# Kernel optimization log

Hardware: AMD Instinct MI355X
Metric: run time of the kernel (lower is better)

The kernel has to match this reference:

```python
import jax, jax.numpy as jnp
import numpy as np

NUM_K = 10
T = 1.0  # softmax temperature (forward default)


def setup_inputs() -> dict:
    key = jax.random.key(0)
    k1, k2, k3, k4 = jax.random.split(key, 4)
    B, H, P, D = 64, 12, 197, 64
    return {
        "att_s": jax.random.normal(k1, (B, H, P, P), dtype=jnp.float32),
        "att_t": jax.random.normal(k2, (B, H, P, P), dtype=jnp.float32),
        "v_s": jax.random.normal(k3, (B, H, P, D), dtype=jnp.float32),
        "v_t": jax.random.normal(k4, (B, H, P, D), dtype=jnp.float32),
    }


def _topk_masked_attend(att, v):
    # att: [B,H,P,P] logits, v: [B,H,P,D]
    a = jax.nn.softmax(att / T, axis=-1)
    # kth-largest value per row acts as the threshold (torch.topk semantics)
    margin = jax.lax.top_k(a, NUM_K)[0][..., -1]           # [B,H,P]
    a = a * (a >= margin[..., None])                        # keep top-k entries
    norm = a.sum(-1)                                        # [B,H,P]
    return jnp.einsum("bhpq,bhqd->bhpd", a, v) / norm[..., None]


def reference(att_s, att_t, v_s, v_t):
    out_s = _topk_masked_attend(att_s, v_s)
    out_t = _topk_masked_attend(att_t, v_t)
    # nn.MSELoss default reduction='mean'
    return jnp.mean(jnp.square(out_s - out_t))
```

## Files before the change

kernel.cpp:

```cpp
#include <hip/hip_runtime.h>
#include <cstdint>
#include <cfloat>

#define NK 10
constexpr int Pp   = 197;
constexpr int Dd   = 64;
constexpr int ROWS = 64 * 12 * 197;
constexpr int BLK  = 256;
constexpr int RPB  = 256;
constexpr int NBLK = ROWS / RPB;
constexpr int CH   = 32;
constexpr int NFULL = Pp / CH;
constexpr int TAIL  = Pp - NFULL * CH;
constexpr float INV_N = 1.0f / 9682944.0f;

__device__ __forceinline__ uint32_t fbits(float x) { return __float_as_uint(x); }
__device__ __forceinline__ float    bfl(uint32_t u) { return __uint_as_float(u); }

template <int CW>
__device__ __forceinline__ void consume_chunk(const float* __restrict__ trow,
                                              float a[NK]) {
#pragma unroll
  for (int j = 0; j < CW; ++j) {
    float x = trow[j];
#pragma unroll
    for (int s = 0; s < NK - 1; ++s) a[s] = fmaxf(a[s], fminf(x, a[s + 1]));
    a[NK - 1] = fmaxf(a[NK - 1], x);
  }
}

__device__ __forceinline__ void load_chunk_regs(const float* __restrict__ slab,
                                                int c, int t, float pf[CH]) {
  if (c < NFULL) {
    const int r0 = t >> 5, j = t & 31;
    const uint32_t col = (uint32_t)(c * CH + j);
    const float* p = slab + c * CH + r0 * Pp + j;
#pragma unroll
    for (int i = 0; i < CH; ++i) {
      float x = p[i * 8 * Pp];
      pf[i] = bfl((fbits(x) & 0xFFFFFF00u) | col);
    }
  } else {
    const float* cbase = slab + NFULL * CH;
#pragma unroll
    for (int i = 0; i < TAIL; ++i) {
      int e = t + i * BLK;
      int r = e / TAIL, j = e % TAIL;
      float x = cbase[r * Pp + j];
      pf[i] = bfl((fbits(x) & 0xFFFFFF00u) | (uint32_t)(NFULL * CH + j));
    }
  }
}

__device__ __forceinline__ void store_chunk(float (*tile)[CH + 1], int c, int t,
                                            const float pf[CH]) {
  if (c < NFULL) {
    const int r0 = t >> 5, j = t & 31;
#pragma unroll
    for (int i = 0; i < CH; ++i) tile[r0 + 8 * i][j] = pf[i];
  } else {
#pragma unroll
    for (int i = 0; i < TAIL; ++i) {
      int e = t + i * BLK;
      tile[e / TAIL][e % TAIL] = pf[i];
    }
  }
}

__device__ __forceinline__ void select_rows(const float* __restrict__ A,
                                            float (*tile)[CH + 1],
                                            float wsel[NK], int t,
                                            int blockRow0) {
  float a[NK];
#pragma unroll
  for (int k = 0; k < NK; ++k) a[k] = -FLT_MAX;

  const float* slab = A + (size_t)blockRow0 * Pp;
  float pf[CH];

  load_chunk_regs(slab, 0, t, pf);
  for (int c = 0; c <= NFULL; ++c) {
    __syncthreads();
    store_chunk(tile, c, t, pf);
    __syncthreads();
    if (c < NFULL) {
      load_chunk_regs(slab, c + 1, t, pf);
      consume_chunk<CH>(tile[t], a);
    } else {
      consume_chunk<TAIL>(tile[t], a);
    }
  }

  float mx = a[NK - 1];
  float e[NK], s = 0.f;
#pragma unroll
  for (int k = 0; k < NK; ++k) {
    e[k] = __expf(a[k] - mx);
    s += e[k];
  }
  float inv = 1.0f / s;
#pragma unroll
  for (int k = 0; k < NK; ++k) {
    float w = e[k] * inv;
    wsel[k] = bfl((fbits(w) & 0xFFFFFF00u) | (fbits(a[k]) & 0xFFu));
  }
}

__global__ __launch_bounds__(BLK, 4) void topk_mse_kernel(
    const float* __restrict__ att_s, const float* __restrict__ att_t,
    const float* __restrict__ v_s, const float* __restrict__ v_t,
    float* __restrict__ out) {
  __shared__ float tile[RPB][CH + 1];
  __shared__ float red[BLK / 64];

  const int t = threadIdx.x;
  const int blockRow0 = blockIdx.x * RPB;

  float wsel[2][NK];
  select_rows(att_s, tile, wsel[0], t, blockRow0);
  select_rows(att_t, tile, wsel[1], t, blockRow0);

  const int wv = t >> 6, l = t & 63;
  float accsum = 0.f;
  for (int i = 0; i < 64; ++i) {
    int rl = (wv << 6) | i;
    int rg = blockRow0 + rl;
    int bh = rg / Pp;
    const float* vsb = v_s + (size_t)bh * (Pp * Dd) + l;
    const float* vtb = v_t + (size_t)bh * (Pp * Dd) + l;
    float acc = 0.f;
#pragma unroll
    for (int k = 0; k < NK; ++k) {
      float w = __shfl(wsel[0][k], i, 64);
      int idx = (int)(fbits(w) & 0xFFu);
      acc = fmaf(w, vsb[idx * Dd], acc);
    }
#pragma unroll
    for (int k = 0; k < NK; ++k) {
      float w = __shfl(wsel[1][k], i, 64);
      int idx = (int)(fbits(w) & 0xFFu);
      acc = fmaf(-w, vtb[idx * Dd], acc);
    }
    accsum = fmaf(acc, acc, accsum);
  }

#pragma unroll
  for (int off = 32; off > 0; off >>= 1) accsum += __shfl_xor(accsum, off, 64);
  if (l == 0) red[wv] = accsum;
  __syncthreads();
  if (t == 0) {
    float tot = (red[0] + red[1]) + (red[2] + red[3]);
    atomicAdd(out, tot * INV_N);
  }
}

extern "C" void kernel_launch(void* const* d_in, const int* in_sizes, int n_in,
                              void* d_out, int out_size, void* d_ws,
                              size_t ws_size, hipStream_t stream) {
  const float* att_s = (const float*)d_in[0];
  const float* att_t = (const float*)d_in[1];
  const float* v_s = (const float*)d_in[2];
  const float* v_t = (const float*)d_in[3];
  float* out = (float*)d_out;

  hipMemsetAsync(out, 0, sizeof(float), stream);
  topk_mse_kernel<<<NBLK, BLK, 0, stream>>>(att_s, att_t, v_s, v_t, out);
}
```

Before: 385.6 us.

## Split fused kernel into select, gather, and reduce kernels with workspace

The single fused kernel is split into three. A select kernel gets one block per slab per tensor, doubling the grid, and writes packed top-k weights and indices to a workspace. A gather kernel assigns one wave per row to fetch the V rows and write per-block partial sums, and a final single-block reduce kernel replaces the atomicAdd and memset. The attention loads are also marked nontemporal. The split is meant to raise parallelism and drop the serial per-wave 64-row gather loop, at the cost of extra launches and a workspace write and read.

```diff
diff --git a/kernel.cpp b/kernel.cpp
--- a/kernel.cpp
+++ b/kernel.cpp
@@ -13,6 +13,9 @@
 constexpr int NFULL = Pp / CH;
 constexpr int TAIL  = Pp - NFULL * CH;
 constexpr float INV_N = 1.0f / 9682944.0f;
+
+constexpr int RPB_B = 16;
+constexpr int NB_B  = ROWS / RPB_B;
 
 __device__ __forceinline__ uint32_t fbits(float x) { return __float_as_uint(x); }
 __device__ __forceinline__ float    bfl(uint32_t u) { return __uint_as_float(u); }
@@ -37,7 +40,7 @@
     const float* p = slab + c * CH + r0 * Pp + j;
 #pragma unroll
     for (int i = 0; i < CH; ++i) {
-      float x = p[i * 8 * Pp];
+      float x = __builtin_nontemporal_load(&p[i * 8 * Pp]);
       pf[i] = bfl((fbits(x) & 0xFFFFFF00u) | col);
     }
   } else {
@@ -46,7 +49,7 @@
     for (int i = 0; i < TAIL; ++i) {
       int e = t + i * BLK;
       int r = e / TAIL, j = e % TAIL;
-      float x = cbase[r * Pp + j];
+      float x = __builtin_nontemporal_load(&cbase[r * Pp + j]);
       pf[i] = bfl((fbits(x) & 0xFFFFFF00u) | (uint32_t)(NFULL * CH + j));
     }
   }
@@ -67,24 +70,32 @@
   }
 }
 
-__device__ __forceinline__ void select_rows(const float* __restrict__ A,
-                                            float (*tile)[CH + 1],
-                                            float wsel[NK], int t,
-                                            int blockRow0) {
+__global__ __launch_bounds__(BLK, 4) void select_kernel(
+    const float* __restrict__ att_s, const float* __restrict__ att_t,
+    float* __restrict__ wpk ) {
+  __shared__ float tile[RPB][CH + 1];
+
+  const int t = threadIdx.x;
+  const int bi = blockIdx.x;
+  const int tensor = (bi >= NBLK) ? 1 : 0;
+  const int slab = bi - tensor * NBLK;
+  const float* A = tensor ? att_t : att_s;
+  const int blockRow0 = slab * RPB;
+
   float a[NK];
 #pragma unroll
   for (int k = 0; k < NK; ++k) a[k] = -FLT_MAX;
 
-  const float* slab = A + (size_t)blockRow0 * Pp;
+  const float* slabp = A + (size_t)blockRow0 * Pp;
   float pf[CH];
 
-  load_chunk_regs(slab, 0, t, pf);
+  load_chunk_regs(slabp, 0, t, pf);
   for (int c = 0; c <= NFULL; ++c) {
     __syncthreads();
     store_chunk(tile, c, t, pf);
     __syncthreads();
     if (c < NFULL) {
-      load_chunk_regs(slab, c + 1, t, pf);
+      load_chunk_regs(slabp, c + 1, t, pf);
       consume_chunk<CH>(tile[t], a);
     } else {
       consume_chunk<TAIL>(tile[t], a);
@@ -94,63 +105,77 @@
   float mx = a[NK - 1];
   float e[NK], s = 0.f;
 #pragma unroll
-  for (int k = 0; k < NK; ++k) {
-    e[k] = __expf(a[k] - mx);
-    s += e[k];
-  }
+  for (int k = 0; k < NK; ++k) { e[k] = __expf(a[k] - mx); s += e[k]; }
   float inv = 1.0f / s;
+
+  __syncthreads();
+  float* flat = &tile[0][0];
 #pragma unroll
   for (int k = 0; k < NK; ++k) {
     float w = e[k] * inv;
-    wsel[k] = bfl((fbits(w) & 0xFFFFFF00u) | (fbits(a[k]) & 0xFFu));
+    flat[t * NK + k] = bfl((fbits(w) & 0xFFFFFF00u) | (fbits(a[k]) & 0xFFu));
+  }
+  __syncthreads();
+  float* dst = wpk + ((size_t)tensor * ROWS + blockRow0) * NK;
+#pragma unroll
+  for (int i = 0; i < NK; ++i) dst[t + i * BLK] = flat[t + i * BLK];
+}
+
+__global__ __launch_bounds__(1024) void gather_kernel(
+    const float* __restrict__ v_s, const float* __restrict__ v_t,
+    const float* __restrict__ wpk, float* __restrict__ partial) {
+  const int t = threadIdx.x, wv = t >> 6, l = t & 63;
+  int row = blockIdx.x * RPB_B + wv;
+  row = __builtin_amdgcn_readfirstlane(row);
+  const int bh = row / Pp;
+  const float* vsb = v_s + (size_t)bh * (Pp * Dd) + l;
+  const float* vtb = v_t + (size_t)bh * (Pp * Dd) + l;
+  const float* w0 = wpk + (size_t)row * NK;
+  const float* w1 = wpk + ((size_t)ROWS + row) * NK;
+
+  float acc = 0.f;
+#pragma unroll
+  for (int k = 0; k < NK; ++k) {
+    float w = w0[k];
+    int idx = (int)(fbits(w) & 0xFFu);
+    acc = fmaf(w, vsb[idx * Dd], acc);
+  }
+#pragma unroll
+  for (int k = 0; k < NK; ++k) {
+    float w = w1[k];
+    int idx = (int)(fbits(w) & 0xFFu);
+    acc = fmaf(-w, vtb[idx * Dd], acc);
+  }
+  float sq = acc * acc;
+#pragma unroll
+  for (int off = 32; off > 0; off >>= 1) sq += __shfl_xor(sq, off, 64);
+
+  __shared__ float red[RPB_B];
+  if (l == 0) red[wv] = sq;
+  __syncthreads();
+  if (t == 0) {
+    float tot = 0.f;
+#pragma unroll
+    for (int i = 0; i < RPB_B; ++i) tot += red[i];
+    partial[blockIdx.x] = tot;
   }
 }
 
-__global__ __launch_bounds__(BLK, 4) void topk_mse_kernel(
-    const float* __restrict__ att_s, const float* __restrict__ att_t,
-    const float* __restrict__ v_s, const float* __restrict__ v_t,
-    float* __restrict__ out) {
-  __shared__ float tile[RPB][CH + 1];
-  __shared__ float red[BLK / 64];
-
-  const int t = threadIdx.x;
-  const int blockRow0 = blockIdx.x * RPB;
-
-  float wsel[2][NK];
-  select_rows(att_s, tile, wsel[0], t, blockRow0);
-  select_rows(att_t, tile, wsel[1], t, blockRow0);
-
-  const int wv = t >> 6, l = t & 63;
-  float accsum = 0.f;
-  for (int i = 0; i < 64; ++i) {
-    int rl = (wv << 6) | i;
-    int rg = blockRow0 + rl;
-    int bh = rg / Pp;
-    const float* vsb = v_s + (size_t)bh * (Pp * Dd) + l;
-    const float* vtb = v_t + (size_t)bh * (Pp * Dd) + l;
-    float acc = 0.f;
+__global__ __launch_bounds__(1024) void reduce_kernel(
+    const float* __restrict__ partial, float* __restrict__ out) {
+  const int t = threadIdx.x, wv = t >> 6, l = t & 63;
+  float s = 0.f;
+  for (int i = t; i < NB_B; i += 1024) s += partial[i];
 #pragma unroll
-    for (int k = 0; k < NK; ++k) {
-      float w = __shfl(wsel[0][k], i, 64);
-      int idx = (int)(fbits(w) & 0xFFu);
-      acc = fmaf(w, vsb[idx * Dd], acc);
-    }
-#pragma unroll
-    for (int k = 0; k < NK; ++k) {
-      float w = __shfl(wsel[1][k], i, 64);
-      int idx = (int)(fbits(w) & 0xFFu);
-      acc = fmaf(-w, vtb[idx * Dd], acc);
-    }
-    accsum = fmaf(acc, acc, accsum);
-  }
-
-#pragma unroll
-  for (int off = 32; off > 0; off >>= 1) accsum += __shfl_xor(accsum, off, 64);
-  if (l == 0) red[wv] = accsum;
+  for (int off = 32; off > 0; off >>= 1) s += __shfl_xor(s, off, 64);
+  __shared__ float red[16];
+  if (l == 0) red[wv] = s;
   __syncthreads();
   if (t == 0) {
-    float tot = (red[0] + red[1]) + (red[2] + red[3]);
-    atomicAdd(out, tot * INV_N);
+    float tot = 0.f;
+#pragma unroll
+    for (int i = 0; i < 16; ++i) tot += red[i];
+    out[0] = tot * INV_N;
   }
 }
 
@@ -163,6 +188,10 @@
   const float* v_t = (const float*)d_in[3];
   float* out = (float*)d_out;
 
-  hipMemsetAsync(out, 0, sizeof(float), stream);
-  topk_mse_kernel<<<NBLK, BLK, 0, stream>>>(att_s, att_t, v_s, v_t, out);
+  float* wpk = (float*)d_ws;
+  float* partial = wpk + (size_t)2 * ROWS * NK;
+
+  select_kernel<<<2 * NBLK, BLK, 0, stream>>>(att_s, att_t, wpk);
+  gather_kernel<<<NB_B, 1024, 0, stream>>>(v_s, v_t, wpk, partial);
+  reduce_kernel<<<1, 1024, 0, stream>>>(partial, out);
 }
```

New measurement: 379.0 us. Within noise of the previous version (-1.7%).
